# Performance work log

Hardware: AMD Instinct MI355X
Metric: run time of the kernel (lower is better)

## Reference

```python
import jax, jax.numpy as jnp
import numpy as np

B, L, H, NH = 32, 200, 64, 2
HS = H // NH
NEG = -2.0**32 + 1.0  # matches torch paddings = -2**32 + 1


def _split_heads(x):
    # torch: cat(split(x, HS, dim=2), dim=0) -> [(h b) l d], head varies slowest
    b, l, _ = x.shape
    return x.reshape(b, l, NH, HS).transpose(2, 0, 1, 3).reshape(NH * b, l, HS)


def setup_inputs() -> dict:
    key = jax.random.key(0)
    ks = jax.random.split(key, 12)
    s = 1.0 / np.sqrt(H)
    return {
        "queries": jax.random.normal(ks[0], (B, L, H), jnp.float32),
        "keys": jax.random.normal(ks[1], (B, L, H), jnp.float32),
        "values": jax.random.normal(ks[2], (B, L, H), jnp.float32),
        "time_matrix_K": jax.random.normal(ks[3], (NH * B, L, L, H), jnp.float32),
        "time_mask": jax.random.bernoulli(ks[4], 0.1, (B, L)),  # True = padded query position
        "attn_mask": jnp.triu(jnp.ones((L, L), bool), k=1),      # True = masked (causal)
        "Wq": jax.random.normal(ks[5], (H, H), jnp.float32) * s,
        "bq": jnp.zeros((H,), jnp.float32),
        "Wk": jax.random.normal(ks[6], (H, H), jnp.float32) * s,
        "bk": jnp.zeros((H,), jnp.float32),
        "Wv": jax.random.normal(ks[7], (H, H), jnp.float32) * s,
        "bv": jnp.zeros((H,), jnp.float32),
        "Wt": jax.random.normal(ks[8], (H, H), jnp.float32) * s,
        "bt": jnp.zeros((H,), jnp.float32),
        "Wp": jax.random.normal(ks[9], (H, 1), jnp.float32) * s,
        "bp": jnp.zeros((1,), jnp.float32),
    }


def reference(queries, keys, values, time_matrix_K, time_mask, attn_mask,
              Wq, bq, Wk, bk, Wv, bv, Wt, bt, Wp, bp):
    Q = queries @ Wq + bq
    K = keys @ Wk + bk
    V = values @ Wv + bv
    Q_ = _split_heads(Q)   # [hB, L, HS]
    K_ = _split_heads(K)
    V_ = _split_heads(V)

    attn = jnp.einsum('bqd,bkd->bqk', Q_, K_)  # [hB, L, L]
    # time bias: Linear -> ReLU -> Linear(->1) -> sigmoid -> squeeze
    tw = jax.nn.sigmoid((jax.nn.relu(time_matrix_K @ Wt + bt) @ Wp + bp)[..., 0])  # [hB, L, L]
    # note: log-bias added BEFORE scaling, as in the original
    attn = (attn + jnp.log(tw)) / jnp.sqrt(jnp.asarray(HS, attn.dtype))

    tm = jnp.tile(time_mask, (NH, 1))[:, :, None]      # [hB, L, 1] -> broadcast over keys
    mask = tm | attn_mask[None, :, :]                  # [hB, L, L]
    attn = jnp.where(mask, jnp.asarray(NEG, attn.dtype), attn)
    attn = jax.nn.softmax(attn, axis=-1)
    # dropout is identity in eval/deterministic mode

    out = jnp.einsum('bqk,bkd->bqd', attn, V_)         # [hB, L, HS]
    # torch: cat(split(out, B, dim=0), dim=2) -> [B, L, H]
    out = out.reshape(NH, B, L, HS).transpose(1, 2, 0, 3).reshape(B, L, H)
    return out, attn
```

## Files before the change

kernel.cpp:

```cpp
#include <hip/hip_runtime.h>
#include <math.h>

#define BB 32
#define LL 200
#define HH 64
#define HSS 32
#define HB 64
#define TRI (LL*(LL+1)/2)
#define ROWS 512
#define NEGV (-4294967295.0f)

typedef __bf16 bf16x8 __attribute__((ext_vector_type(8)));
typedef float f32x4 __attribute__((ext_vector_type(4)));

__global__ __launch_bounds__(64) void proj_kernel(
    const float* __restrict__ q_in, const float* __restrict__ k_in,
    const float* __restrict__ v_in,
    const float* __restrict__ Wq, const float* __restrict__ bq,
    const float* __restrict__ Wk, const float* __restrict__ bk,
    const float* __restrict__ Wv, const float* __restrict__ bv,
    const float* __restrict__ Wt, unsigned short* __restrict__ WtT,
    float* __restrict__ Qs, float* __restrict__ Ks, float* __restrict__ Vs)
{
    const int row = blockIdx.x;
    const int b = row / LL, l = row % LL;
    const int j = threadIdx.x;

    if (blockIdx.x < 64) {
        const int t = blockIdx.x*64 + j;
        const int n = t >> 6, k = t & 63;
        const __bf16 h = (__bf16)Wt[k*HH + n];
        WtT[t] = __builtin_bit_cast(unsigned short, h);
    }

    __shared__ float s[3][HH];
    s[0][j] = q_in[row*HH + j];
    s[1][j] = k_in[row*HH + j];
    s[2][j] = v_in[row*HH + j];
    __syncthreads();

    const float* W[3]    = {Wq, Wk, Wv};
    const float* bias[3] = {bq, bk, bv};
    float*       dst[3]  = {Qs, Ks, Vs};

    const int hb  = (j >> 5)*BB + b;
    const int idx = (hb*LL + l)*HSS + (j & 31);

    #pragma unroll
    for (int m = 0; m < 3; ++m) {
        float acc = bias[m][j];
        #pragma unroll
        for (int i = 0; i < HH; ++i)
            acc = fmaf(s[m][i], W[m][i*HH + j], acc);
        dst[m][idx] = acc;
    }
}

__global__ __launch_bounds__(256) void mlp_kernel(
    const float* __restrict__ T,
    const unsigned short* __restrict__ WtT,
    const float* __restrict__ bt, const float* __restrict__ Wp,
    float* __restrict__ Plog)
{
    const int hb   = blockIdx.y;
    const int r0   = blockIdx.x * ROWS;
    const int tid  = threadIdx.x;
    const int wave = tid >> 6;
    const int lane = tid & 63;
    const int bl   = lane & 15;
    const int bg   = lane >> 4;

    __shared__ __align__(16) unsigned short sA[2][64*HH];
    __shared__ int sBase[ROWS];

    #pragma unroll
    for (int j = 0; j < ROWS/256; ++j) {
        int r = r0 + j*256 + tid;
        if (r >= TRI) r = TRI - 1;
        const float s = sqrtf((float)(8*r + 1));
        int qq = (int)((s - 1.0f) * 0.5f);
        while ((qq + 1)*(qq + 2)/2 <= r) ++qq;
        while (qq*(qq + 1)/2 > r) --qq;
        const int kk = r - qq*(qq + 1)/2;
        sBase[j*256 + tid] = ((hb*LL + qq)*LL + kk) << 4;
    }
    __syncthreads();

    const float4* T4 = reinterpret_cast<const float4*>(T);

#define LOADCHUNK(CUR, c)                                                      \
    {                                                                          \
        _Pragma("unroll")                                                      \
        for (int i = 0; i < 4; ++i) {                                          \
            const int g = i*256 + tid;                                         \
            CUR[i] = T4[sBase[(c)*64 + (g >> 4)] + (g & 15)];                  \
        }                                                                      \
    }

    float4 va[4], vb[4];
    LOADCHUNK(va, 0)
    LOADCHUNK(vb, 1)

    bf16x8 bfrag[4][2];
    float  btv[4], wpv[4];
    #pragma unroll
    for (int n = 0; n < 4; ++n) {
        #pragma unroll
        for (int k = 0; k < 2; ++k) {
            const uint4 raw = *reinterpret_cast<const uint4*>(
                WtT + ((n*16 + bl)*HH + k*32 + bg*8));
            bfrag[n][k] = __builtin_bit_cast(bf16x8, raw);
        }
        btv[n] = bt[n*16 + bl];
        wpv[n] = Wp[n*16 + bl];
    }

#define PACK_ISSUE_COMPUTE(c, CUR, DO_ISSUE, NC)                               \
    {                                                                          \
                     \
        _Pragma("unroll")                                                      \
        for (int i = 0; i < 4; ++i) {                                          \
            const int g = i*256 + tid;                                         \
            const int row = g >> 4, cf4 = g & 15;                              \
            union { __bf16 h[4]; uint2 u2; } pk;                               \
            pk.h[0] = (__bf16)CUR[i].x; pk.h[1] = (__bf16)CUR[i].y;            \
            pk.h[2] = (__bf16)CUR[i].z; pk.h[3] = (__bf16)CUR[i].w;            \
            const int byteoff = row*128 + ((cf4*8) ^ ((row & 7) << 4));        \
            *reinterpret_cast<uint2*>(                                         \
                reinterpret_cast<char*>(sA[(c) & 1]) + byteoff) = pk.u2;       \
        }                                                                      \
        if (DO_ISSUE) LOADCHUNK(CUR, NC)          \
           \
        asm volatile("s_waitcnt lgkmcnt(0)" ::: "memory");                     \
        __builtin_amdgcn_s_barrier();                                          \
                                                                               \
        const int arow = wave*16 + bl;                                         \
        bf16x8 afrag[2];                                                       \
        _Pragma("unroll")                                                      \
        for (int k = 0; k < 2; ++k) {                                          \
            const int abyte = arow*128 + ((k*64 + bg*16) ^ ((arow & 7) << 4)); \
            const uint4 raw = *reinterpret_cast<const uint4*>(                 \
                reinterpret_cast<const char*>(sA[(c) & 1]) + abyte);           \
            afrag[k] = __builtin_bit_cast(bf16x8, raw);                        \
        }                                                                      \
        f32x4 acc[4];                                                          \
        _Pragma("unroll")                                                      \
        for (int n = 0; n < 4; ++n) {                                          \
            acc[n] = (f32x4){0.f, 0.f, 0.f, 0.f};                              \
            acc[n] = __builtin_amdgcn_mfma_f32_16x16x32_bf16(                  \
                         afrag[0], bfrag[n][0], acc[n], 0, 0, 0);              \
            acc[n] = __builtin_amdgcn_mfma_f32_16x16x32_bf16(                  \
                         afrag[1], bfrag[n][1], acc[n], 0, 0, 0);              \
        }                                                                      \
        float p[4] = {0.f, 0.f, 0.f, 0.f};                                     \
        _Pragma("unroll")                                                      \
        for (int n = 0; n < 4; ++n) {                                          \
            _Pragma("unroll")                                                  \
            for (int r = 0; r < 4; ++r)                                        \
                p[r] = fmaf(fmaxf(acc[n][r] + btv[n], 0.f), wpv[n], p[r]);     \
        }                                                                      \
        _Pragma("unroll")                                                      \
        for (int m = 1; m < 16; m <<= 1) {                                     \
            _Pragma("unroll")                                                  \
            for (int r = 0; r < 4; ++r) p[r] += __shfl_xor(p[r], m, 64);       \
        }                                                                      \
        if (bl == 0) {                                                         \
            _Pragma("unroll")                                                  \
            for (int r = 0; r < 4; ++r) {                                      \
                const int lr = (c)*64 + wave*16 + bg*4 + r;                    \
                if (r0 + lr < TRI)                                             \
                    Plog[sBase[lr] >> 4] = p[r];       \
            }                                                                  \
        }                                                                      \
    }

    PACK_ISSUE_COMPUTE(0, va, 1, 2)
    PACK_ISSUE_COMPUTE(1, vb, 1, 3)
    PACK_ISSUE_COMPUTE(2, va, 1, 4)
    PACK_ISSUE_COMPUTE(3, vb, 1, 5)
    PACK_ISSUE_COMPUTE(4, va, 1, 6)
    PACK_ISSUE_COMPUTE(5, vb, 1, 7)
    PACK_ISSUE_COMPUTE(6, va, 0, 0)
    PACK_ISSUE_COMPUTE(7, vb, 0, 0)
#undef PACK_ISSUE_COMPUTE
#undef LOADCHUNK
}

__global__ __launch_bounds__(256) void attn2_kernel(
    const float* __restrict__ Qs, const float* __restrict__ Ks,
    const float* __restrict__ Vs,
    const int*   __restrict__ time_mask,
    const float* __restrict__ bp,
    float* __restrict__ out, float* __restrict__ attn_out )
{
    const int q    = blockIdx.x;
    const int hb   = blockIdx.y;
    const int b    = hb & (BB-1);
    const int head = hb >> 5;
    const int tid  = threadIdx.x;
    const int wave = tid >> 6;
    const int lane = tid & 63;

    __shared__ float sQ[HSS];
    __shared__ float sLogit[LL];
    __shared__ float sRed[8];
    __shared__ float sO[8][HSS];

    const bool qmask = (time_mask[b*LL + q] != 0);
    const bool live  = (tid < LL) && !qmask && (tid <= q);

    float pv = 0.0f;
    if (live) pv = attn_out[((size_t)hb*LL + q)*LL + tid];

    if (tid < HSS) sQ[tid] = Qs[(hb*LL + q)*HSS + tid];
    const float bp0 = bp[0];
    const float scale = 0.17677669529663687f;
    __syncthreads();

    if (tid < LL) {
        float logit = NEGV;
        if (live) {
            const float4* kr = reinterpret_cast<const float4*>(
                Ks + (hb*LL + tid)*HSS);
            float qk = 0.0f;
            #pragma unroll
            for (int i = 0; i < 8; ++i) {
                const float4 kv = kr[i];
                qk += kv.x*sQ[4*i+0] + kv.y*sQ[4*i+1]
                    + kv.z*sQ[4*i+2] + kv.w*sQ[4*i+3];
            }
            const float x  = pv + bp0;
            const float ls = -logf(1.0f + expf(-x));
            logit = (qk + ls) * scale;
        }
        sLogit[tid] = logit;
    }
    __syncthreads();

    const float v = (tid < LL) ? sLogit[tid] : -INFINITY;
    float mx = v;
    #pragma unroll
    for (int s = 1; s < 64; s <<= 1) mx = fmaxf(mx, __shfl_xor(mx, s, 64));
    if (lane == 0) sRed[wave] = mx;
    __syncthreads();
    const float rowmax = fmaxf(fmaxf(sRed[0], sRed[1]), fmaxf(sRed[2], sRed[3]));

    const float e = (tid < LL) ? expf(v - rowmax) : 0.0f;
    float sm = e;
    #pragma unroll
    for (int s = 1; s < 64; s <<= 1) sm += __shfl_xor(sm, s, 64);
    if (lane == 0) sRed[4 + wave] = sm;
    __syncthreads();
    const float rowsum = sRed[4] + sRed[5] + sRed[6] + sRed[7];
    const float a = e * (1.0f / rowsum);

    __syncthreads();
    if (tid < LL) {
        sLogit[tid] = a;
        attn_out[((size_t)hb*LL + q)*LL + tid] = a;
    }
    __syncthreads();

    {
        const int d = tid & 31;
        const int g = tid >> 5;
        float acc = 0.0f;
        for (int k = g*25; k < g*25 + 25; ++k)
            acc = fmaf(sLogit[k], Vs[(hb*LL + k)*HSS + d], acc);
        sO[g][d] = acc;
        __syncthreads();
        if (tid < HSS) {
            float o = 0.0f;
            #pragma unroll
            for (int g2 = 0; g2 < 8; ++g2) o += sO[g2][tid];
            out[((size_t)b*LL + q)*HH + head*HSS + tid] = o;
        }
    }
}

extern "C" void kernel_launch(void* const* d_in, const int* in_sizes, int n_in,
                              void* d_out, int out_size, void* d_ws, size_t ws_size,
                              hipStream_t stream) {
    const float* queries = (const float*)d_in[0];
    const float* keys    = (const float*)d_in[1];
    const float* values  = (const float*)d_in[2];
    const float* T       = (const float*)d_in[3];
    const int*   tmask   = (const int*)d_in[4];
    const float* Wq = (const float*)d_in[6];
    const float* bq = (const float*)d_in[7];
    const float* Wk = (const float*)d_in[8];
    const float* bk = (const float*)d_in[9];
    const float* Wv = (const float*)d_in[10];
    const float* bv = (const float*)d_in[11];
    const float* Wt = (const float*)d_in[12];
    const float* bt = (const float*)d_in[13];
    const float* Wp = (const float*)d_in[14];
    const float* bp = (const float*)d_in[15];

    float* Qs = (float*)d_ws;
    float* Ks = Qs + HB*LL*HSS;
    float* Vs = Ks + HB*LL*HSS;
    unsigned short* WtT = (unsigned short*)(Vs + HB*LL*HSS);

    float* out      = (float*)d_out;
    float* attn_out = out + BB*LL*HH;

    proj_kernel<<<BB*LL, 64, 0, stream>>>(queries, keys, values,
                                          Wq, bq, Wk, bk, Wv, bv,
                                          Wt, WtT, Qs, Ks, Vs);

    dim3 mgrid((TRI + ROWS - 1) / ROWS, HB);
    mlp_kernel<<<mgrid, 256, 0, stream>>>(T, WtT, bt, Wp, attn_out);

    dim3 agrid(LL, HB);
    attn2_kernel<<<agrid, 256, 0, stream>>>(Qs, Ks, Vs, tmask, bp,
                                            out, attn_out);
}
```

Baseline: 119.5 us.

## Process two query rows per attention block and enlarge MLP row tiles

```diff
diff --git a/kernel.cpp b/kernel.cpp
--- a/kernel.cpp
+++ b/kernel.cpp
@@ -7,7 +7,7 @@
 #define HSS 32
 #define HB 64
 #define TRI (LL*(LL+1)/2)
-#define ROWS 512
+#define ROWS 640
 #define NEGV (-4294967295.0f)
 
 typedef __bf16 bf16x8 __attribute__((ext_vector_type(8)));
@@ -74,15 +74,18 @@
     __shared__ int sBase[ROWS];
 
     #pragma unroll
-    for (int j = 0; j < ROWS/256; ++j) {
-        int r = r0 + j*256 + tid;
-        if (r >= TRI) r = TRI - 1;
-        const float s = sqrtf((float)(8*r + 1));
-        int qq = (int)((s - 1.0f) * 0.5f);
-        while ((qq + 1)*(qq + 2)/2 <= r) ++qq;
-        while (qq*(qq + 1)/2 > r) --qq;
-        const int kk = r - qq*(qq + 1)/2;
-        sBase[j*256 + tid] = ((hb*LL + qq)*LL + kk) << 4;
+    for (int j = 0; j < 3; ++j) {
+        const int rr = j*256 + tid;
+        if (rr < ROWS) {
+            int r = r0 + rr;
+            if (r >= TRI) r = TRI - 1;
+            const float s = sqrtf((float)(8*r + 1));
+            int qq = (int)((s - 1.0f) * 0.5f);
+            while ((qq + 1)*(qq + 2)/2 <= r) ++qq;
+            while (qq*(qq + 1)/2 > r) --qq;
+            const int kk = r - qq*(qq + 1)/2;
+            sBase[rr] = ((hb*LL + qq)*LL + kk) << 4;
+        }
     }
     __syncthreads();
 
@@ -180,8 +183,10 @@
     PACK_ISSUE_COMPUTE(3, vb, 1, 5)
     PACK_ISSUE_COMPUTE(4, va, 1, 6)
     PACK_ISSUE_COMPUTE(5, vb, 1, 7)
-    PACK_ISSUE_COMPUTE(6, va, 0, 0)
-    PACK_ISSUE_COMPUTE(7, vb, 0, 0)
+    PACK_ISSUE_COMPUTE(6, va, 1, 8)
+    PACK_ISSUE_COMPUTE(7, vb, 1, 9)
+    PACK_ISSUE_COMPUTE(8, va, 0, 0)
+    PACK_ISSUE_COMPUTE(9, vb, 0, 0)
 #undef PACK_ISSUE_COMPUTE
 #undef LOADCHUNK
 }
@@ -193,7 +198,8 @@
     const float* __restrict__ bp,
     float* __restrict__ out, float* __restrict__ attn_out )
 {
-    const int q    = blockIdx.x;
+    const int q0   = blockIdx.x;
+    const int q1   = q0 + 100;
     const int hb   = blockIdx.y;
     const int b    = hb & (BB-1);
     const int head = hb >> 5;
@@ -201,79 +207,111 @@
     const int wave = tid >> 6;
     const int lane = tid & 63;
 
-    __shared__ float sQ[HSS];
-    __shared__ float sLogit[LL];
-    __shared__ float sRed[8];
-    __shared__ float sO[8][HSS];
-
-    const bool qmask = (time_mask[b*LL + q] != 0);
-    const bool live  = (tid < LL) && !qmask && (tid <= q);
-
-    float pv = 0.0f;
-    if (live) pv = attn_out[((size_t)hb*LL + q)*LL + tid];
-
-    if (tid < HSS) sQ[tid] = Qs[(hb*LL + q)*HSS + tid];
+    __shared__ float sQ[2][HSS];
+    __shared__ float sLogit[2][LL];
+    __shared__ float sRed[2][8];
+    __shared__ float sO[2][8][HSS];
+
+    const bool qm0 = (time_mask[b*LL + q0] != 0);
+    const bool qm1 = (time_mask[b*LL + q1] != 0);
+    const bool live0 = (tid < LL) && !qm0 && (tid <= q0);
+    const bool live1 = (tid < LL) && !qm1 && (tid <= q1);
+
+    float pv0 = 0.0f, pv1 = 0.0f;
+    if (live0) pv0 = attn_out[((size_t)hb*LL + q0)*LL + tid];
+    if (live1) pv1 = attn_out[((size_t)hb*LL + q1)*LL + tid];
+
+    if (tid < 2*HSS)
+        sQ[tid >> 5][tid & 31] =
+            Qs[(hb*LL + ((tid < HSS) ? q0 : q1))*HSS + (tid & 31)];
     const float bp0 = bp[0];
     const float scale = 0.17677669529663687f;
     __syncthreads();
 
     if (tid < LL) {
-        float logit = NEGV;
-        if (live) {
+        float l0 = NEGV, l1 = NEGV;
+        if (live0 || live1) {
             const float4* kr = reinterpret_cast<const float4*>(
                 Ks + (hb*LL + tid)*HSS);
-            float qk = 0.0f;
+            float qk0 = 0.0f, qk1 = 0.0f;
             #pragma unroll
             for (int i = 0; i < 8; ++i) {
                 const float4 kv = kr[i];
-                qk += kv.x*sQ[4*i+0] + kv.y*sQ[4*i+1]
-                    + kv.z*sQ[4*i+2] + kv.w*sQ[4*i+3];
+                qk0 += kv.x*sQ[0][4*i+0] + kv.y*sQ[0][4*i+1]
+                     + kv.z*sQ[0][4*i+2] + kv.w*sQ[0][4*i+3];
+                qk1 += kv.x*sQ[1][4*i+0] + kv.y*sQ[1][4*i+1]
+                     + kv.z*sQ[1][4*i+2] + kv.w*sQ[1][4*i+3];
             }
-            const float x  = pv + bp0;
-            const float ls = -logf(1.0f + expf(-x));
-            logit = (qk + ls) * scale;
-        }
-        sLogit[tid] = logit;
-    }
-    __syncthreads();
-
-    const float v = (tid < LL) ? sLogit[tid] : -INFINITY;
-    float mx = v;
-    #pragma unroll
-    for (int s = 1; s < 64; s <<= 1) mx = fmaxf(mx, __shfl_xor(mx, s, 64));
-    if (lane == 0) sRed[wave] = mx;
-    __syncthreads();
-    const float rowmax = fmaxf(fmaxf(sRed[0], sRed[1]), fmaxf(sRed[2], sRed[3]));
-
-    const float e = (tid < LL) ? expf(v - rowmax) : 0.0f;
-    float sm = e;
-    #pragma unroll
-    for (int s = 1; s < 64; s <<= 1) sm += __shfl_xor(sm, s, 64);
-    if (lane == 0) sRed[4 + wave] = sm;
-    __syncthreads();
-    const float rowsum = sRed[4] + sRed[5] + sRed[6] + sRed[7];
-    const float a = e * (1.0f / rowsum);
-
-    __syncthreads();
+            if (live0) {
+                const float x = pv0 + bp0;
+                l0 = (qk0 - logf(1.0f + expf(-x))) * scale;
+            }
+            if (live1) {
+                const float x = pv1 + bp0;
+                l1 = (qk1 - logf(1.0f + expf(-x))) * scale;
+            }
+        }
+        sLogit[0][tid] = l0;
+        sLogit[1][tid] = l1;
+    }
+    __syncthreads();
+
+    const float v0 = (tid < LL) ? sLogit[0][tid] : -INFINITY;
+    const float v1 = (tid < LL) ? sLogit[1][tid] : -INFINITY;
+    float m0 = v0, m1 = v1;
+    #pragma unroll
+    for (int s = 1; s < 64; s <<= 1) {
+        m0 = fmaxf(m0, __shfl_xor(m0, s, 64));
+        m1 = fmaxf(m1, __shfl_xor(m1, s, 64));
+    }
+    if (lane == 0) { sRed[0][wave] = m0; sRed[1][wave] = m1; }
+    __syncthreads();
+    const float rmax0 = fmaxf(fmaxf(sRed[0][0], sRed[0][1]),
+                              fmaxf(sRed[0][2], sRed[0][3]));
+    const float rmax1 = fmaxf(fmaxf(sRed[1][0], sRed[1][1]),
+                              fmaxf(sRed[1][2], sRed[1][3]));
+
+    const float e0 = (tid < LL) ? expf(v0 - rmax0) : 0.0f;
+    const float e1 = (tid < LL) ? expf(v1 - rmax1) : 0.0f;
+    float s0 = e0, s1 = e1;
+    #pragma unroll
+    for (int s = 1; s < 64; s <<= 1) {
+        s0 += __shfl_xor(s0, s, 64);
+        s1 += __shfl_xor(s1, s, 64);
+    }
+    if (lane == 0) { sRed[0][4 + wave] = s0; sRed[1][4 + wave] = s1; }
+    __syncthreads();
+    const float rsum0 = sRed[0][4] + sRed[0][5] + sRed[0][6] + sRed[0][7];
+    const float rsum1 = sRed[1][4] + sRed[1][5] + sRed[1][6] + sRed[1][7];
+    const float a0 = e0 * (1.0f / rsum0);
+    const float a1 = e1 * (1.0f / rsum1);
+
     if (tid < LL) {
-        sLogit[tid] = a;
-        attn_out[((size_t)hb*LL + q)*LL + tid] = a;
+        sLogit[0][tid] = a0;
+        sLogit[1][tid] = a1;
+        attn_out[((size_t)hb*LL + q0)*LL + tid] = a0;
+        attn_out[((size_t)hb*LL + q1)*LL + tid] = a1;
     }
     __syncthreads();
 
     {
         const int d = tid & 31;
         const int g = tid >> 5;
-        float acc = 0.0f;
-        for (int k = g*25; k < g*25 + 25; ++k)
-            acc = fmaf(sLogit[k], Vs[(hb*LL + k)*HSS + d], acc);
-        sO[g][d] = acc;
+        float acc0 = 0.0f, acc1 = 0.0f;
+        for (int k = g*25; k < g*25 + 25; ++k) {
+            const float vv = Vs[(hb*LL + k)*HSS + d];
+            acc0 = fmaf(sLogit[0][k], vv, acc0);
+            acc1 = fmaf(sLogit[1][k], vv, acc1);
+        }
+        sO[0][g][d] = acc0;
+        sO[1][g][d] = acc1;
         __syncthreads();
-        if (tid < HSS) {
+        if (tid < 2*HSS) {
+            const int which = tid >> 5, d2 = tid & 31;
             float o = 0.0f;
             #pragma unroll
-            for (int g2 = 0; g2 < 8; ++g2) o += sO[g2][tid];
-            out[((size_t)b*LL + q)*HH + head*HSS + tid] = o;
+            for (int g2 = 0; g2 < 8; ++g2) o += sO[which][g2][d2];
+            out[((size_t)b*LL + (which ? q1 : q0))*HH + head*HSS + d2] = o;
         }
     }
 }
@@ -312,7 +350,7 @@
     dim3 mgrid((TRI + ROWS - 1) / ROWS, HB);
     mlp_kernel<<<mgrid, 256, 0, stream>>>(T, WtT, bt, Wp, attn_out);
 
-    dim3 agrid(LL, HB);
+    dim3 agrid(LL/2, HB);
     attn2_kernel<<<agrid, 256, 0, stream>>>(Qs, Ks, Vs, tmask, bp,
                                             out, attn_out);
 }
```

After: 113.3 us (median of 2 runs). -5.3%, faster.
